# Kernel tuning notes

Hardware: AMD Instinct MI355X
Metric: run time of the kernel (lower is better)

Reference implementation:

```python
import jax, jax.numpy as jnp
import numpy as np

DIV_COEF = 1.0
EPS = 1e-8  # torch.cosine_similarity default eps


def setup_inputs() -> dict:
    key = jax.random.key(0)
    id_ = jax.random.normal(key, (8192, 512), dtype=jnp.float32)
    return {"id": id_}


def reference(id):
    # cosine similarity via norm + GEMM (math identical to broadcast form)
    norms = jnp.linalg.norm(id, axis=1)                      # [N]
    dots = id @ id.T                                          # [N, N]
    sim = dots / jnp.maximum(norms[:, None] * norms[None, :], EPS)
    n = id.shape[0]
    # zero diagonal, clamp negatives to zero, mean over full NxN
    off_diag = 1.0 - jnp.eye(n, dtype=sim.dtype)
    id_sim = off_diag * sim
    l_id_div = jnp.mean(jnp.where(id_sim < 0, 0.0, id_sim))
    total_loss = DIV_COEF * l_id_div
    return (total_loss, l_id_div)
```

## Files before the change

### kernel.cpp

```cpp
#include <hip/hip_runtime.h>
#include <stdint.h>

#define NROWS 8192
#define KDIM  512
#define BM    128
#define BK    256
#define NKI   (KDIM / BK)
#define NT    (NROWS / BM)
#define NBLK  (NT * (NT + 1) / 2)

typedef __attribute__((ext_vector_type(4))) float f32x4;
typedef long i64;

__device__ __forceinline__ void async_copy16(const unsigned char* g, unsigned char* l) {
  __builtin_amdgcn_global_load_lds(
      (const __attribute__((address_space(1))) unsigned int*)g,
      (__attribute__((address_space(3))) unsigned int*)l,
      16, 0, 0);
}

__global__ __launch_bounds__(128) void prep_kernel(
    const float* __restrict__ src, unsigned char* __restrict__ dst,
    float* __restrict__ acc) {
  const int row = blockIdx.x;
  const int tid = threadIdx.x;
  const float4 v = ((const float4*)src)[row * 128 + tid];
  float ss = v.x * v.x + v.y * v.y + v.z * v.z + v.w * v.w;
  #pragma unroll
  for (int off = 32; off > 0; off >>= 1) ss += __shfl_down(ss, off);
  __shared__ float red[2];
  __shared__ float s_rn;
  const int lane = tid & 63, w = tid >> 6;
  if (lane == 0) red[w] = ss;
  __syncthreads();
  if (tid == 0) {
    s_rn = 1.0f / sqrtf(red[0] + red[1]);
    if (row == 0) *acc = 0.0f;
  }
  __syncthreads();
  const float rn = s_rn;
  int pk = __builtin_amdgcn_cvt_pk_fp8_f32(v.x * rn, v.y * rn, 0, false);
  pk     = __builtin_amdgcn_cvt_pk_fp8_f32(v.z * rn, v.w * rn, pk, true);
  const int cg  = tid >> 2;
  const int win = cg >> 4;
  const int p   = (cg & 15) ^ (row & 15);
  ((unsigned int*)dst)[row * 128 + win * 64 + p * 4 + (tid & 3)] = (unsigned int)pk;
}

__device__ __forceinline__ int tri_base(int b) {
  return b * NT - (b * (b - 1)) / 2;
}

__global__ __launch_bounds__(256) void sim_reduce_kernel(
    const unsigned char* __restrict__ idn, float* __restrict__ acc) {
  const int idx = blockIdx.x;
  const float Af = 2.0f * NT + 1.0f;
  int bi = (int)((Af - sqrtf(Af * Af - 8.0f * (float)idx)) * 0.5f);
  while (bi > 0 && tri_base(bi) > idx) bi--;
  while (tri_base(bi + 1) <= idx) bi++;
  const int bj = bi + (idx - tri_base(bi));

  __shared__ __align__(16) unsigned char As[BM * BK];
  __shared__ __align__(16) unsigned char Bs[BM * BK];

  const int tid  = threadIdx.x;
  const int lane = tid & 63;
  const int w    = tid >> 6;
  const int wr   = (w >> 1) * 64;
  const int wc   = (w & 1) * 64;
  const int q    = lane >> 4;
  const int r16  = lane & 15;
  const int h8   = (q & 1) * 8;

  f32x4 acc_f[4][4];
  #pragma unroll
  for (int i = 0; i < 4; i++)
    #pragma unroll
    for (int j = 0; j < 4; j++)
      acc_f[i][j] = (f32x4){0.f, 0.f, 0.f, 0.f};

  const unsigned char* gA = idn + (size_t)(bi * BM + (tid >> 4)) * KDIM + (tid & 15) * 16;
  const unsigned char* gB = idn + (size_t)(bj * BM + (tid >> 4)) * KDIM + (tid & 15) * 16;
  unsigned char* lA = As + tid * 16;
  unsigned char* lB = Bs + tid * 16;

  #pragma unroll
  for (int t = 0; t < NKI; ++t) {
    if (t) __syncthreads();
    const int ko = t * BK;
    #pragma unroll
    for (int i = 0; i < 8; i++) async_copy16(gA + ko + i * 8192, lA + i * 4096);
    #pragma unroll
    for (int i = 0; i < 8; i++) async_copy16(gB + ko + i * 8192, lB + i * 4096);
    asm volatile("s_waitcnt vmcnt(0)" ::: "memory");
    __syncthreads();

    #pragma unroll
    for (int s = 0; s < 8; s++) {
      const int pos = ((2 * s + (q >> 1)) ^ r16) * 16 + h8;
      i64 a[4], b[4];
      #pragma unroll
      for (int mi = 0; mi < 4; mi++) {
        a[mi] = *(const i64*)&As[(wr + mi * 16 + r16) * BK + pos];
        b[mi] = *(const i64*)&Bs[(wc + mi * 16 + r16) * BK + pos];
      }
      #pragma unroll
      for (int mi = 0; mi < 4; mi++)
        #pragma unroll
        for (int ni = 0; ni < 4; ni++)
          acc_f[mi][ni] = __builtin_amdgcn_mfma_f32_16x16x32_fp8_fp8(
              a[mi], b[ni], acc_f[mi][ni], 0, 0, 0);
    }
  }

  float local = 0.f;
  const bool diag = (bi == bj);
  #pragma unroll
  for (int mi = 0; mi < 4; mi++)
    #pragma unroll
    for (int ni = 0; ni < 4; ni++)
      #pragma unroll
      for (int rr = 0; rr < 4; rr++) {
        const int ri = wr + mi * 16 + q * 4 + rr;
        const int ci = wc + ni * 16 + r16;
        float v = fmaxf(acc_f[mi][ni][rr], 0.f);
        if (diag && ri == ci) v = 0.f;
        local += v;
      }

  #pragma unroll
  for (int off = 32; off > 0; off >>= 1) local += __shfl_down(local, off);
  __syncthreads();
  float* red = (float*)As;
  if (lane == 0) red[w] = local;
  __syncthreads();
  if (tid == 0) {
    float s = red[0] + red[1] + red[2] + red[3];
    if (!diag) s *= 2.f;
    atomicAdd(acc, s);
  }
}

__global__ void finalize_kernel(const float* __restrict__ acc, float* __restrict__ out) {
  const float m = *acc * (1.0f / ((float)NROWS * (float)NROWS));
  out[0] = m;
  out[1] = m;
}

extern "C" void kernel_launch(void* const* d_in, const int* in_sizes, int n_in,
                              void* d_out, int out_size, void* d_ws, size_t ws_size,
                              hipStream_t stream) {
  const float* id = (const float*)d_in[0];
  float* out = (float*)d_out;
  unsigned char* idn = (unsigned char*)d_ws;
  float* acc = (float*)((char*)d_ws + (size_t)NROWS * KDIM);

  prep_kernel<<<NROWS, 128, 0, stream>>>(id, idn, acc);
  sim_reduce_kernel<<<NBLK, 256, 0, stream>>>(idn, acc);
  finalize_kernel<<<1, 1, 0, stream>>>(acc, out);
}
```

Measured before the change: 103.7 us.

## Use one wave per row in prep and add half-swizzle to fp8 layout

The prep kernel now handles four rows per block with one wavefront per row. Each lane loads two float4s and reduces the norm with shuffles only, so shared memory and __syncthreads are gone. The fp8 output layout gains an extra XOR on the 8-byte half within each 16-byte chunk, and the GEMM kernel's LDS read offsets are changed to match. This is meant to cut LDS bank conflicts on the i64 fragment reads and lower the overhead of the prep launch. The risk is a wrong result if the swizzle is inconsistent between the two kernels.

```diff
diff --git a/kernel.cpp b/kernel.cpp
--- a/kernel.cpp
+++ b/kernel.cpp
@@ -19,32 +19,29 @@
       16, 0, 0);
 }
 
-__global__ __launch_bounds__(128) void prep_kernel(
+__global__ __launch_bounds__(256) void prep_kernel(
     const float* __restrict__ src, unsigned char* __restrict__ dst,
     float* __restrict__ acc) {
-  const int row = blockIdx.x;
-  const int tid = threadIdx.x;
-  const float4 v = ((const float4*)src)[row * 128 + tid];
-  float ss = v.x * v.x + v.y * v.y + v.z * v.z + v.w * v.w;
+  const int row  = blockIdx.x * 4 + (threadIdx.x >> 6);
+  const int lane = threadIdx.x & 63;
+  const float4 v0 = ((const float4*)src)[row * 128 + lane * 2];
+  const float4 v1 = ((const float4*)src)[row * 128 + lane * 2 + 1];
+  float ss = v0.x * v0.x + v0.y * v0.y + v0.z * v0.z + v0.w * v0.w
+           + v1.x * v1.x + v1.y * v1.y + v1.z * v1.z + v1.w * v1.w;
   #pragma unroll
   for (int off = 32; off > 0; off >>= 1) ss += __shfl_down(ss, off);
-  __shared__ float red[2];
-  __shared__ float s_rn;
-  const int lane = tid & 63, w = tid >> 6;
-  if (lane == 0) red[w] = ss;
-  __syncthreads();
-  if (tid == 0) {
-    s_rn = 1.0f / sqrtf(red[0] + red[1]);
-    if (row == 0) *acc = 0.0f;
-  }
-  __syncthreads();
-  const float rn = s_rn;
-  int pk = __builtin_amdgcn_cvt_pk_fp8_f32(v.x * rn, v.y * rn, 0, false);
-  pk     = __builtin_amdgcn_cvt_pk_fp8_f32(v.z * rn, v.w * rn, pk, true);
-  const int cg  = tid >> 2;
+  const float rn = 1.0f / sqrtf(__shfl(ss, 0));
+  if (row == 0 && lane == 0) *acc = 0.0f;
+  int pk0 = __builtin_amdgcn_cvt_pk_fp8_f32(v0.x * rn, v0.y * rn, 0, false);
+  pk0     = __builtin_amdgcn_cvt_pk_fp8_f32(v0.z * rn, v0.w * rn, pk0, true);
+  int pk1 = __builtin_amdgcn_cvt_pk_fp8_f32(v1.x * rn, v1.y * rn, 0, false);
+  pk1     = __builtin_amdgcn_cvt_pk_fp8_f32(v1.z * rn, v1.w * rn, pk1, true);
+  const int cg = lane >> 1;
   const int win = cg >> 4;
-  const int p   = (cg & 15) ^ (row & 15);
-  ((unsigned int*)dst)[row * 128 + win * 64 + p * 4 + (tid & 3)] = (unsigned int)pk;
+  const int p  = (cg & 15) ^ (row & 15);
+  const int hf = (lane & 1) ^ ((row >> 3) & 1);
+  uint2 o; o.x = (unsigned int)pk0; o.y = (unsigned int)pk1;
+  ((uint2*)dst)[row * 64 + win * 32 + p * 2 + hf] = o;
 }
 
 __device__ __forceinline__ int tri_base(int b) {
@@ -70,7 +67,7 @@
   const int wc   = (w & 1) * 64;
   const int q    = lane >> 4;
   const int r16  = lane & 15;
-  const int h8   = (q & 1) * 8;
+  const int hq   = (((q & 1) ^ ((r16 >> 3) & 1))) * 8;
 
   f32x4 acc_f[4][4];
   #pragma unroll
@@ -97,7 +94,7 @@
 
     #pragma unroll
     for (int s = 0; s < 8; s++) {
-      const int pos = ((2 * s + (q >> 1)) ^ r16) * 16 + h8;
+      const int pos = ((2 * s + (q >> 1)) ^ r16) * 16 + hq;
       i64 a[4], b[4];
       #pragma unroll
       for (int mi = 0; mi < 4; mi++) {
@@ -155,7 +152,7 @@
   unsigned char* idn = (unsigned char*)d_ws;
   float* acc = (float*)((char*)d_ws + (size_t)NROWS * KDIM);
 
-  prep_kernel<<<NROWS, 128, 0, stream>>>(id, idn, acc);
+  prep_kernel<<<NROWS / 4, 256, 0, stream>>>(id, idn, acc);
   sim_reduce_kernel<<<NBLK, 256, 0, stream>>>(idn, acc);
   finalize_kernel<<<1, 1, 0, stream>>>(acc, out);
 }
```

Result: faster. 100.5 us (-3.1%).
